# Performance work log

Measured on AMD Instinct MI355X. Metric: run time of the kernel, lower is better.

Reference implementation:

```python
import jax, jax.numpy as jnp
import numpy as np

HEAD_NUM = 16
QKV_DIM = 16
EMB = 256
MS_HID = 16
B, R, C = 4, 512, 512


def setup_inputs() -> dict:
    key = jax.random.key(0)
    ks = jax.random.split(key, 10)
    inv = 1.0 / np.sqrt(EMB)
    m1 = np.sqrt(0.5)
    m2 = np.sqrt(1.0 / 16.0)
    return {
        "row_emb": jax.random.normal(ks[0], (B, R, EMB), jnp.float32),
        "col_emb": jax.random.normal(ks[1], (B, C, EMB), jnp.float32),
        "cost_mat": jax.random.uniform(ks[2], (B, R, C), jnp.float32),
        # Linear(no bias) weights stored as [in, out] so y = x @ W
        "Wq": jax.random.uniform(ks[3], (EMB, HEAD_NUM * QKV_DIM), jnp.float32, -inv, inv),
        "Wk": jax.random.uniform(ks[4], (EMB, HEAD_NUM * QKV_DIM), jnp.float32, -inv, inv),
        "Wv": jax.random.uniform(ks[5], (EMB, HEAD_NUM * QKV_DIM), jnp.float32, -inv, inv),
        "mix1_weight": jax.random.uniform(ks[6], (HEAD_NUM, 2, MS_HID), jnp.float32, -m1, m1),
        "mix1_bias": jax.random.uniform(ks[7], (HEAD_NUM, MS_HID), jnp.float32, -m1, m1),
        "mix2_weight": jax.random.uniform(ks[8], (HEAD_NUM, MS_HID, 1), jnp.float32, -m2, m2),
        "mix2_bias": jax.random.uniform(ks[9], (HEAD_NUM, 1), jnp.float32, -m2, m2),
    }


def _split_heads(x):
    # [b, g, h*s] -> [b, h, g, s]
    b, g, _ = x.shape
    return x.reshape(b, g, HEAD_NUM, QKV_DIM).transpose(0, 2, 1, 3)


def reference(row_emb, col_emb, cost_mat, Wq, Wk, Wv, mix1_weight, mix1_bias, mix2_weight, mix2_bias):
    q = _split_heads(row_emb @ Wq)  # [b,h,r,s]
    k = _split_heads(col_emb @ Wk)  # [b,h,c,s]
    v = _split_heads(col_emb @ Wv)  # [b,h,c,s]

    dot = jnp.einsum("bhrs,bhcs->bhrc", q, k) / jnp.sqrt(jnp.float32(QKV_DIM))
    cost = jnp.broadcast_to(cost_mat[:, None, :, :], dot.shape)
    two = jnp.stack((dot, cost), axis=-1)  # [b,h,r,c,2]

    # per-head 2-layer MLP applied to each (row, col) score pair
    ms1 = jnp.einsum("bhrcx,hxm->bhrcm", two, mix1_weight) + mix1_bias[None, :, None, None, :]
    ms1 = jax.nn.relu(ms1)
    mixed = jnp.einsum("bhrcm,hmo->bhrco", ms1, mix2_weight)[..., 0] + mix2_bias[None, :, None, None, 0]

    weights = jax.nn.softmax(mixed, axis=3)  # [b,h,r,c]
    out = jnp.einsum("bhrc,bhcs->bhrs", weights, v)
    b, h, r, s = out.shape
    return out.transpose(0, 2, 1, 3).reshape(b, r, h * s)
```

## Files before the change

kernel.cpp:

```cpp
#include <hip/hip_runtime.h>

#define NB 4
#define NH 16
#define RR 512
#define CC 512
#define EMB 256
#define SD 16
#define MH 16

typedef __attribute__((ext_vector_type(8))) short short8;
typedef __attribute__((ext_vector_type(8))) unsigned short ushort8;
typedef __attribute__((ext_vector_type(4))) float f32x4;
typedef __attribute__((ext_vector_type(4))) unsigned short ushort4v;

__device__ __forceinline__ float bf2f(unsigned short s) {
  unsigned u = ((unsigned)s) << 16;
  return __builtin_bit_cast(float, u);
}
__device__ __forceinline__ unsigned short f2bf(float f) {
  unsigned u = __builtin_bit_cast(unsigned, f);
  u = u + 0x7FFFu + ((u >> 16) & 1u);
  return (unsigned short)(u >> 16);
}

__global__ __launch_bounds__(256) void prep_w(
    const float* __restrict__ Wq, const float* __restrict__ Wk,
    const float* __restrict__ Wv, unsigned short* __restrict__ WT) {
  int bi = blockIdx.x;
  int mat = bi >> 4, ngrp = bi & 15;
  const float* src = (mat == 0) ? Wq : (mat == 1) ? Wk : Wv;
  unsigned short* dst = WT + mat * (EMB * EMB);
  int n = ngrp * 16 + (threadIdx.x >> 4);
  int e0 = (threadIdx.x & 15) * 16;
  ushort8 v0, v1;
#pragma unroll
  for (int j = 0; j < 8; ++j) v0[j] = f2bf(src[(e0 + j) * EMB + n]);
#pragma unroll
  for (int j = 0; j < 8; ++j) v1[j] = f2bf(src[(e0 + 8 + j) * EMB + n]);
  *(ushort8*)(dst + n * EMB + e0) = v0;
  *(ushort8*)(dst + n * EMB + e0 + 8) = v1;
}

__global__ __launch_bounds__(256) void proj_kernel(
    const float* __restrict__ rowe, const float* __restrict__ cole,
    const unsigned short* __restrict__ WT,
    unsigned short* __restrict__ Q, unsigned short* __restrict__ K,
    unsigned short* __restrict__ VT) {
  int tid = threadIdx.x;
  int wid = tid >> 6, lane = tid & 63, l15 = lane & 15, quad = lane >> 4;
  int wt = blockIdx.x * 4 + wid;
  int mat = wt >> 9;
  int t = wt & 511;
  int rt = t >> 2, ng = t & 3;
  const float* X = (mat == 0) ? rowe : cole;
  const unsigned short* Wm = WT + mat * (EMB * EMB);
  const float* xrow = X + (size_t)(rt * 16 + l15) * EMB + quad * 8;

  short8 xf[8];
#pragma unroll
  for (int e = 0; e < 8; ++e) {
    f32x4 b0 = *(const f32x4*)(xrow + e * 32);
    f32x4 b1 = *(const f32x4*)(xrow + e * 32 + 4);
#pragma unroll
    for (int j = 0; j < 4; ++j) {
      ((unsigned short*)&xf[e])[j]     = f2bf(b0[j]);
      ((unsigned short*)&xf[e])[j + 4] = f2bf(b1[j]);
    }
  }
  int row = rt * 16 + l15;
  int b = row >> 9, loc = row & 511;
#pragma unroll
  for (int hh = 0; hh < 4; ++hh) {
    int nt = ng * 4 + hh;
    const short8* ap = (const short8*)(Wm + (nt * 16 + l15) * EMB + quad * 8);
    f32x4 acc = {0.f, 0.f, 0.f, 0.f};
#pragma unroll
    for (int e = 0; e < 8; ++e)
      acc = __builtin_amdgcn_mfma_f32_16x16x32_bf16(ap[e * 4], xf[e], acc, 0, 0, 0);
    if (mat < 2) {
      ushort4v pk;
      pk.x = f2bf(acc[0]); pk.y = f2bf(acc[1]); pk.z = f2bf(acc[2]); pk.w = f2bf(acc[3]);
      unsigned short* dst = ((mat == 0) ? Q : K) +
          ((size_t)((b * NH + nt) * 512 + loc) * SD + quad * 4);
      *(ushort4v*)dst = pk;
    } else {
#pragma unroll
      for (int i = 0; i < 4; ++i)
        VT[(size_t)((b * NH + nt) * SD + quad * 4 + i) * CC + loc] = f2bf(acc[i]);
    }
  }
}

__global__ __launch_bounds__(256) void attn_kernel(
    const unsigned short* __restrict__ Q, const unsigned short* __restrict__ K,
    const unsigned short* __restrict__ VT, const float* __restrict__ cost,
    const float* __restrict__ m1w, const float* __restrict__ m1b,
    const float* __restrict__ m2w, const float* __restrict__ m2b,
    float* __restrict__ out) {
  __shared__ alignas(16) unsigned short Psh[4][16 * 256];
  __shared__ float Osh[2][256];
  __shared__ float MLsh[2][2][2][16];
  int tid = threadIdx.x;
  int wid = tid >> 6, lane = tid & 63, l15 = lane & 15, quad = lane >> 4;
  int rt = wid >> 1, ch = wid & 1;
  int rb = blockIdx.x, h = blockIdx.y, b = blockIdx.z;
  int bh = b * NH + h;
  int r0 = rb * 32 + rt * 16;
  int cbase = ch * 256;

  float wa[MH], wc[MH], wd[MH], we[MH];
#pragma unroll
  for (int m = 0; m < MH; ++m) {
    wa[m] = m1w[(h * 2 + 0) * MH + m] * 0.25f;
    wc[m] = m1w[(h * 2 + 1) * MH + m];
    wd[m] = m1b[h * MH + m];
    we[m] = m2w[h * MH + m];
  }
  float wb2 = m2b[h];

  short8 qf = {0, 0, 0, 0, 0, 0, 0, 0};
  const unsigned short* Qb = Q + (size_t)bh * RR * SD;
  if (quad < 2) qf = *(const short8*)(Qb + (r0 + l15) * SD + quad * 8);

  const unsigned short* Kb = K + ((size_t)bh * CC + cbase) * SD;
  const float* crow = cost + ((size_t)b * RR + r0 + l15) * CC + cbase;
  unsigned short* psrow = &Psh[wid][l15 * 256];

  float mrun = -1e30f;
  short8 kf_c = {0, 0, 0, 0, 0, 0, 0, 0};
  if (quad < 2) kf_c = *(const short8*)(Kb + l15 * SD + quad * 8);
  f32x4 cf_c = *(const f32x4*)(crow + quad * 4);
#pragma unroll 4
  for (int it = 0; it < 16; ++it) {
    int itn = (it + 1) & 15;
    short8 kf_n = {0, 0, 0, 0, 0, 0, 0, 0};
    if (quad < 2) kf_n = *(const short8*)(Kb + (itn * 16 + l15) * SD + quad * 8);
    f32x4 cf_n = *(const f32x4*)(crow + itn * 16 + quad * 4);

    f32x4 acc = {0.f, 0.f, 0.f, 0.f};
    acc = __builtin_amdgcn_mfma_f32_16x16x32_bf16(kf_c, qf, acc, 0, 0, 0);
    int c0 = it * 16 + quad * 4;
    ushort4v pk;
#pragma unroll
    for (int i = 0; i < 4; ++i) {
      float x = acc[i];
      float s = wb2;
#pragma unroll
      for (int m = 0; m < MH; ++m) {
        float t1 = fmaf(wc[m], cf_c[i], wd[m]);
        t1 = fmaf(wa[m], x, t1);
        t1 = fmaxf(t1, 0.f);
        s = fmaf(we[m], t1, s);
      }
      mrun = fmaxf(mrun, s);
      ((unsigned short*)&pk)[i] = f2bf(s);
    }
    int g = ((c0 >> 3) ^ (l15 & 7));
    *(ushort4v*)(psrow + g * 8 + (c0 & 7)) = pk;
    kf_c = kf_n; cf_c = cf_n;
  }
  mrun = fmaxf(mrun, __shfl_xor(mrun, 16));
  mrun = fmaxf(mrun, __shfl_xor(mrun, 32));

  const unsigned short* vb = VT + ((size_t)bh * SD + l15) * CC + cbase;
  f32x4 o = {0.f, 0.f, 0.f, 0.f};
  float lsum = 0.f;
  const float L2E = 1.44269504088896f;
  float mb2 = mrun * L2E;
  short8 vf_c = *(const short8*)(vb + quad * 8);
  int g0 = ((quad * 8) >> 3) ^ (l15 & 7);
  short8 pr_c = *(const short8*)(psrow + g0 * 8);
#pragma unroll
  for (int it = 0; it < 8; ++it) {
    int itn = (it + 1) & 7;
    short8 vf_n = *(const short8*)(vb + itn * 32 + quad * 8);
    int c0n = itn * 32 + quad * 8;
    int gn = ((c0n >> 3) ^ (l15 & 7));
    short8 pr_n = *(const short8*)(psrow + gn * 8);
    short8 pf;
#pragma unroll
    for (int j = 0; j < 8; ++j) {
      float x = bf2f(((unsigned short*)&pr_c)[j]);
      float p = __builtin_amdgcn_exp2f(fmaf(x, L2E, -mb2));
      lsum += p;
      ((unsigned short*)&pf)[j] = (short)f2bf(p);
    }
    o = __builtin_amdgcn_mfma_f32_16x16x32_bf16(pf, vf_c, o, 0, 0, 0);
    vf_c = vf_n; pr_c = pr_n;
  }
  lsum += __shfl_xor(lsum, 16);
  lsum += __shfl_xor(lsum, 32);

  if (quad == 0) { MLsh[rt][ch][0][l15] = mrun; MLsh[rt][ch][1][l15] = lsum; }
  if (ch == 1) {
#pragma unroll
    for (int i = 0; i < 4; ++i) Osh[rt][(quad * 4 + i) * 16 + l15] = o[i];
  }
  __syncthreads();
  if (ch == 0) {
#pragma unroll
    for (int i = 0; i < 4; ++i) {
      int r = quad * 4 + i;
      float m0 = MLsh[rt][0][0][r], l0 = MLsh[rt][0][1][r];
      float m1 = MLsh[rt][1][0][r], l1 = MLsh[rt][1][1][r];
      float M = fmaxf(m0, m1);
      float a0 = __builtin_amdgcn_exp2f((m0 - M) * L2E);
      float a1 = __builtin_amdgcn_exp2f((m1 - M) * L2E);
      float l = a0 * l0 + a1 * l1;
      float val = (a0 * o[i] + a1 * Osh[rt][r * 16 + l15]) / l;
      out[((size_t)b * RR + r0 + r) * (NH * SD) + h * SD + l15] = val;
    }
  }
}

extern "C" void kernel_launch(void* const* d_in, const int* in_sizes, int n_in,
                              void* d_out, int out_size, void* d_ws, size_t ws_size,
                              hipStream_t stream) {
  const float* rowe = (const float*)d_in[0];
  const float* cole = (const float*)d_in[1];
  const float* cost = (const float*)d_in[2];
  const float* Wq   = (const float*)d_in[3];
  const float* Wk   = (const float*)d_in[4];
  const float* Wv   = (const float*)d_in[5];
  const float* m1w  = (const float*)d_in[6];
  const float* m1b  = (const float*)d_in[7];
  const float* m2w  = (const float*)d_in[8];
  const float* m2b  = (const float*)d_in[9];
  float* outp = (float*)d_out;

  unsigned short* ws = (unsigned short*)d_ws;
  unsigned short* Qw  = ws;
  unsigned short* Kw  = ws + 524288;
  unsigned short* VTw = ws + 1048576;
  unsigned short* WTw = ws + 1572864;

  prep_w<<<dim3(48, 1, 1), 256, 0, stream>>>(Wq, Wk, Wv, WTw);
  proj_kernel<<<dim3(384, 1, 1), 256, 0, stream>>>(rowe, cole, WTw, Qw, Kw, VTw);
  attn_kernel<<<dim3(16, NH, NB), 256, 0, stream>>>(Qw, Kw, VTw, cost,
                                                    m1w, m1b, m2w, m2b, outp);
}
```

Before: 125.7 us.

## Switch pipeline to fp16 and compute per-pair MLP with packed half2 math

Replaces bf16 storage and MFMA with fp16 throughout, using hardware pack-convert instructions instead of manual bf16 rounding. The main change evaluates the per-head score MLP in packed half2 FMA/max with fdot2 accumulation, roughly halving the VALU instruction count of the dominant inner loop. It also drops the quad<2 guards on K loads. The trade-off is fp16 range and precision limits and round-toward-zero conversion in the MLP hidden activations.

```diff
diff --git a/kernel.cpp b/kernel.cpp
--- a/kernel.cpp
+++ b/kernel.cpp
@@ -8,44 +8,37 @@
 #define SD 16
 #define MH 16
 
-typedef __attribute__((ext_vector_type(8))) short short8;
-typedef __attribute__((ext_vector_type(8))) unsigned short ushort8;
 typedef __attribute__((ext_vector_type(4))) float f32x4;
-typedef __attribute__((ext_vector_type(4))) unsigned short ushort4v;
-
-__device__ __forceinline__ float bf2f(unsigned short s) {
-  unsigned u = ((unsigned)s) << 16;
-  return __builtin_bit_cast(float, u);
-}
-__device__ __forceinline__ unsigned short f2bf(float f) {
-  unsigned u = __builtin_bit_cast(unsigned, f);
-  u = u + 0x7FFFu + ((u >> 16) & 1u);
-  return (unsigned short)(u >> 16);
-}
+typedef __fp16 half2v __attribute__((ext_vector_type(2)));
+typedef __fp16 half4v __attribute__((ext_vector_type(4)));
+typedef __fp16 half8v __attribute__((ext_vector_type(8)));
+
+union H8 { half8v v; half2v h[4]; __fp16 e[8]; };
+union H4 { half4v v; half2v h[2]; __fp16 e[4]; };
 
 __global__ __launch_bounds__(256) void prep_w(
     const float* __restrict__ Wq, const float* __restrict__ Wk,
-    const float* __restrict__ Wv, unsigned short* __restrict__ WT) {
+    const float* __restrict__ Wv, __fp16* __restrict__ WT) {
   int bi = blockIdx.x;
   int mat = bi >> 4, ngrp = bi & 15;
   const float* src = (mat == 0) ? Wq : (mat == 1) ? Wk : Wv;
-  unsigned short* dst = WT + mat * (EMB * EMB);
+  __fp16* dst = WT + mat * (EMB * EMB);
   int n = ngrp * 16 + (threadIdx.x >> 4);
   int e0 = (threadIdx.x & 15) * 16;
-  ushort8 v0, v1;
-#pragma unroll
-  for (int j = 0; j < 8; ++j) v0[j] = f2bf(src[(e0 + j) * EMB + n]);
-#pragma unroll
-  for (int j = 0; j < 8; ++j) v1[j] = f2bf(src[(e0 + 8 + j) * EMB + n]);
-  *(ushort8*)(dst + n * EMB + e0) = v0;
-  *(ushort8*)(dst + n * EMB + e0 + 8) = v1;
+  H8 v0, v1;
+#pragma unroll
+  for (int j = 0; j < 8; ++j) v0.e[j] = (__fp16)src[(e0 + j) * EMB + n];
+#pragma unroll
+  for (int j = 0; j < 8; ++j) v1.e[j] = (__fp16)src[(e0 + 8 + j) * EMB + n];
+  *(half8v*)(dst + n * EMB + e0) = v0.v;
+  *(half8v*)(dst + n * EMB + e0 + 8) = v1.v;
 }
 
 __global__ __launch_bounds__(256) void proj_kernel(
     const float* __restrict__ rowe, const float* __restrict__ cole,
-    const unsigned short* __restrict__ WT,
-    unsigned short* __restrict__ Q, unsigned short* __restrict__ K,
-    unsigned short* __restrict__ VT) {
+    const __fp16* __restrict__ WT,
+    __fp16* __restrict__ Q, __fp16* __restrict__ K,
+    __fp16* __restrict__ VT) {
   int tid = threadIdx.x;
   int wid = tid >> 6, lane = tid & 63, l15 = lane & 15, quad = lane >> 4;
   int wt = blockIdx.x * 4 + wid;
@@ -53,51 +46,53 @@
   int t = wt & 511;
   int rt = t >> 2, ng = t & 3;
   const float* X = (mat == 0) ? rowe : cole;
-  const unsigned short* Wm = WT + mat * (EMB * EMB);
+  const __fp16* Wm = WT + mat * (EMB * EMB);
   const float* xrow = X + (size_t)(rt * 16 + l15) * EMB + quad * 8;
 
-  short8 xf[8];
+  half8v xf[8];
 #pragma unroll
   for (int e = 0; e < 8; ++e) {
     f32x4 b0 = *(const f32x4*)(xrow + e * 32);
     f32x4 b1 = *(const f32x4*)(xrow + e * 32 + 4);
-#pragma unroll
-    for (int j = 0; j < 4; ++j) {
-      ((unsigned short*)&xf[e])[j]     = f2bf(b0[j]);
-      ((unsigned short*)&xf[e])[j + 4] = f2bf(b1[j]);
-    }
+    H8 x;
+    x.h[0] = __builtin_amdgcn_cvt_pkrtz(b0[0], b0[1]);
+    x.h[1] = __builtin_amdgcn_cvt_pkrtz(b0[2], b0[3]);
+    x.h[2] = __builtin_amdgcn_cvt_pkrtz(b1[0], b1[1]);
+    x.h[3] = __builtin_amdgcn_cvt_pkrtz(b1[2], b1[3]);
+    xf[e] = x.v;
   }
   int row = rt * 16 + l15;
   int b = row >> 9, loc = row & 511;
 #pragma unroll
   for (int hh = 0; hh < 4; ++hh) {
     int nt = ng * 4 + hh;
-    const short8* ap = (const short8*)(Wm + (nt * 16 + l15) * EMB + quad * 8);
+    const half8v* ap = (const half8v*)(Wm + (nt * 16 + l15) * EMB + quad * 8);
     f32x4 acc = {0.f, 0.f, 0.f, 0.f};
 #pragma unroll
     for (int e = 0; e < 8; ++e)
-      acc = __builtin_amdgcn_mfma_f32_16x16x32_bf16(ap[e * 4], xf[e], acc, 0, 0, 0);
+      acc = __builtin_amdgcn_mfma_f32_16x16x32_f16(ap[e * 4], xf[e], acc, 0, 0, 0);
     if (mat < 2) {
-      ushort4v pk;
-      pk.x = f2bf(acc[0]); pk.y = f2bf(acc[1]); pk.z = f2bf(acc[2]); pk.w = f2bf(acc[3]);
-      unsigned short* dst = ((mat == 0) ? Q : K) +
+      H4 pk;
+      pk.h[0] = __builtin_amdgcn_cvt_pkrtz(acc[0], acc[1]);
+      pk.h[1] = __builtin_amdgcn_cvt_pkrtz(acc[2], acc[3]);
+      __fp16* dst = ((mat == 0) ? Q : K) +
           ((size_t)((b * NH + nt) * 512 + loc) * SD + quad * 4);
-      *(ushort4v*)dst = pk;
+      *(half4v*)dst = pk.v;
     } else {
 #pragma unroll
       for (int i = 0; i < 4; ++i)
-        VT[(size_t)((b * NH + nt) * SD + quad * 4 + i) * CC + loc] = f2bf(acc[i]);
+        VT[(size_t)((b * NH + nt) * SD + quad * 4 + i) * CC + loc] = (__fp16)acc[i];
     }
   }
 }
 
 __global__ __launch_bounds__(256) void attn_kernel(
-    const unsigned short* __restrict__ Q, const unsigned short* __restrict__ K,
-    const unsigned short* __restrict__ VT, const float* __restrict__ cost,
+    const __fp16* __restrict__ Q, const __fp16* __restrict__ K,
+    const __fp16* __restrict__ VT, const float* __restrict__ cost,
     const float* __restrict__ m1w, const float* __restrict__ m1b,
     const float* __restrict__ m2w, const float* __restrict__ m2b,
     float* __restrict__ out) {
-  __shared__ alignas(16) unsigned short Psh[4][16 * 256];
+  __shared__ alignas(16) __fp16 Psh[4][16 * 256];
   __shared__ float Osh[2][256];
   __shared__ float MLsh[2][2][2][16];
   int tid = threadIdx.x;
@@ -108,84 +103,94 @@
   int r0 = rb * 32 + rt * 16;
   int cbase = ch * 256;
 
-  float wa[MH], wc[MH], wd[MH], we[MH];
-#pragma unroll
-  for (int m = 0; m < MH; ++m) {
-    wa[m] = m1w[(h * 2 + 0) * MH + m] * 0.25f;
-    wc[m] = m1w[(h * 2 + 1) * MH + m];
-    wd[m] = m1b[h * MH + m];
-    we[m] = m2w[h * MH + m];
+  half2v wa2[8], wc2[8], wd2[8], we2[8];
+#pragma unroll
+  for (int mp = 0; mp < 8; ++mp) {
+    wa2[mp] = half2v{(__fp16)(m1w[(h * 2 + 0) * MH + 2 * mp] * 0.25f),
+                     (__fp16)(m1w[(h * 2 + 0) * MH + 2 * mp + 1] * 0.25f)};
+    wc2[mp] = half2v{(__fp16)m1w[(h * 2 + 1) * MH + 2 * mp],
+                     (__fp16)m1w[(h * 2 + 1) * MH + 2 * mp + 1]};
+    wd2[mp] = half2v{(__fp16)m1b[h * MH + 2 * mp],
+                     (__fp16)m1b[h * MH + 2 * mp + 1]};
+    we2[mp] = half2v{(__fp16)m2w[h * MH + 2 * mp],
+                     (__fp16)m2w[h * MH + 2 * mp + 1]};
   }
   float wb2 = m2b[h];
-
-  short8 qf = {0, 0, 0, 0, 0, 0, 0, 0};
-  const unsigned short* Qb = Q + (size_t)bh * RR * SD;
-  if (quad < 2) qf = *(const short8*)(Qb + (r0 + l15) * SD + quad * 8);
-
-  const unsigned short* Kb = K + ((size_t)bh * CC + cbase) * SD;
+  const half2v hz2 = {(__fp16)0.f, (__fp16)0.f};
+
+  half8v qf = {0, 0, 0, 0, 0, 0, 0, 0};
+  const __fp16* Qb = Q + (size_t)bh * RR * SD;
+  if (quad < 2) qf = *(const half8v*)(Qb + (r0 + l15) * SD + quad * 8);
+
+  const __fp16* Kb = K + ((size_t)bh * CC + cbase) * SD;
   const float* crow = cost + ((size_t)b * RR + r0 + l15) * CC + cbase;
-  unsigned short* psrow = &Psh[wid][l15 * 256];
+  __fp16* psrow = &Psh[wid][l15 * 256];
 
   float mrun = -1e30f;
-  short8 kf_c = {0, 0, 0, 0, 0, 0, 0, 0};
-  if (quad < 2) kf_c = *(const short8*)(Kb + l15 * SD + quad * 8);
+  half8v kf_c = *(const half8v*)(Kb + l15 * SD + quad * 8);
   f32x4 cf_c = *(const f32x4*)(crow + quad * 4);
 #pragma unroll 4
   for (int it = 0; it < 16; ++it) {
     int itn = (it + 1) & 15;
-    short8 kf_n = {0, 0, 0, 0, 0, 0, 0, 0};
-    if (quad < 2) kf_n = *(const short8*)(Kb + (itn * 16 + l15) * SD + quad * 8);
+    half8v kf_n = *(const half8v*)(Kb + (itn * 16 + l15) * SD + quad * 8);
     f32x4 cf_n = *(const f32x4*)(crow + itn * 16 + quad * 4);
 
     f32x4 acc = {0.f, 0.f, 0.f, 0.f};
-    acc = __builtin_amdgcn_mfma_f32_16x16x32_bf16(kf_c, qf, acc, 0, 0, 0);
+    acc = __builtin_amdgcn_mfma_f32_16x16x32_f16(kf_c, qf, acc, 0, 0, 0);
     int c0 = it * 16 + quad * 4;
-    ushort4v pk;
+    float sv[4];
 #pragma unroll
     for (int i = 0; i < 4; ++i) {
-      float x = acc[i];
+      half2v x2 = __builtin_amdgcn_cvt_pkrtz(acc[i], acc[i]);
+      half2v c2 = __builtin_amdgcn_cvt_pkrtz(cf_c[i], cf_c[i]);
       float s = wb2;
 #pragma unroll
-      for (int m = 0; m < MH; ++m) {
-        float t1 = fmaf(wc[m], cf_c[i], wd[m]);
-        t1 = fmaf(wa[m], x, t1);
-        t1 = fmaxf(t1, 0.f);
-        s = fmaf(we[m], t1, s);
+      for (int mp = 0; mp < 8; ++mp) {
+        half2v t1 = __builtin_elementwise_fma(wc2[mp], c2, wd2[mp]);
+        t1 = __builtin_elementwise_fma(wa2[mp], x2, t1);
+        t1 = __builtin_elementwise_max(t1, hz2);
+        s = __builtin_amdgcn_fdot2(we2[mp], t1, s, false);
       }
+      sv[i] = s;
       mrun = fmaxf(mrun, s);
-      ((unsigned short*)&pk)[i] = f2bf(s);
-    }
+    }
+    H4 pk;
+    pk.h[0] = __builtin_amdgcn_cvt_pkrtz(sv[0], sv[1]);
+    pk.h[1] = __builtin_amdgcn_cvt_pkrtz(sv[2], sv[3]);
     int g = ((c0 >> 3) ^ (l15 & 7));
-    *(ushort4v*)(psrow + g * 8 + (c0 & 7)) = pk;
+    *(half4v*)(psrow + g * 8 + (c0 & 7)) = pk.v;
     kf_c = kf_n; cf_c = cf_n;
   }
   mrun = fmaxf(mrun, __shfl_xor(mrun, 16));
   mrun = fmaxf(mrun, __shfl_xor(mrun, 32));
 
-  const unsigned short* vb = VT + ((size_t)bh * SD + l15) * CC + cbase;
+  const __fp16* vb = VT + ((size_t)bh * SD + l15) * CC + cbase;
   f32x4 o = {0.f, 0.f, 0.f, 0.f};
   float lsum = 0.f;
   const float L2E = 1.44269504088896f;
   float mb2 = mrun * L2E;
-  short8 vf_c = *(const short8*)(vb + quad * 8);
+  half8v vf_c = *(const half8v*)(vb + quad * 8);
   int g0 = ((quad * 8) >> 3) ^ (l15 & 7);
-  short8 pr_c = *(const short8*)(psrow + g0 * 8);
+  H8 pr_c; pr_c.v = *(const half8v*)(psrow + g0 * 8);
 #pragma unroll
   for (int it = 0; it < 8; ++it) {
     int itn = (it + 1) & 7;
-    short8 vf_n = *(const short8*)(vb + itn * 32 + quad * 8);
+    half8v vf_n = *(const half8v*)(vb + itn * 32 + quad * 8);
     int c0n = itn * 32 + quad * 8;
     int gn = ((c0n >> 3) ^ (l15 & 7));
-    short8 pr_n = *(const short8*)(psrow + gn * 8);
-    short8 pf;
+    H8 pr_n; pr_n.v = *(const half8v*)(psrow + gn * 8);
+    float p[8];
 #pragma unroll
     for (int j = 0; j < 8; ++j) {
-      float x = bf2f(((unsigned short*)&pr_c)[j]);
-      float p = __builtin_amdgcn_exp2f(fmaf(x, L2E, -mb2));
-      lsum += p;
-      ((unsigned short*)&pf)[j] = (short)f2bf(p);
-    }
-    o = __builtin_amdgcn_mfma_f32_16x16x32_bf16(pf, vf_c, o, 0, 0, 0);
+      float x = (float)pr_c.e[j];
+      p[j] = __builtin_amdgcn_exp2f(fmaf(x, L2E, -mb2));
+      lsum += p[j];
+    }
+    H8 pf;
+#pragma unroll
+    for (int jj = 0; jj < 4; ++jj)
+      pf.h[jj] = __builtin_amdgcn_cvt_pkrtz(p[2 * jj], p[2 * jj + 1]);
+    o = __builtin_amdgcn_mfma_f32_16x16x32_f16(pf.v, vf_c, o, 0, 0, 0);
     vf_c = vf_n; pr_c = pr_n;
   }
   lsum += __shfl_xor(lsum, 16);
@@ -228,11 +233,11 @@
   const float* m2b  = (const float*)d_in[9];
   float* outp = (float*)d_out;
 
-  unsigned short* ws = (unsigned short*)d_ws;
-  unsigned short* Qw  = ws;
-  unsigned short* Kw  = ws + 524288;
-  unsigned short* VTw = ws + 1048576;
-  unsigned short* WTw = ws + 1572864;
+  __fp16* ws = (__fp16*)d_ws;
+  __fp16* Qw  = ws;
+  __fp16* Kw  = ws + 524288;
+  __fp16* VTw = ws + 1048576;
+  __fp16* WTw = ws + 1572864;
 
   prep_w<<<dim3(48, 1, 1), 256, 0, stream>>>(Wq, Wk, Wv, WTw);
   proj_kernel<<<dim3(384, 1, 1), 256, 0, stream>>>(rowe, cole, WTw, Qw, Kw, VTw);
```

After: 117.6 us. 1.07x faster.
